# Optimization experiments

Hardware: AMD Instinct MI355X
Metric: run time of the kernel (lower is better)

## Reference

```python
import jax, jax.numpy as jnp
import numpy as np

B, T, I, H, O = 64, 2048, 128, 256, 1

def setup_inputs() -> dict:
    key = jax.random.key(0)
    ks = jax.random.split(key, 7)
    s = 0.05
    return {
        "x": jax.random.normal(ks[0], (B, T, I), jnp.float32),
        "W_ih": jax.random.normal(ks[1], (3 * H, I), jnp.float32) * s,
        "W_hh": jax.random.normal(ks[2], (3 * H, H), jnp.float32) * s,
        "b_ih": jax.random.normal(ks[3], (3 * H,), jnp.float32) * s,
        "b_hh": jax.random.normal(ks[4], (3 * H,), jnp.float32) * s,
        "W_o": jax.random.normal(ks[5], (O, H), jnp.float32) * s,
        "b_o": jax.random.normal(ks[6], (O,), jnp.float32) * s,
    }

def _gru_scan(x, W_ih, W_hh, b_ih, b_hh):
    # Precompute input projections for all timesteps: [T, B, 3H]
    gi = jnp.einsum('bti,gi->tbg', x, W_ih) + b_ih
    Hd = W_hh.shape[1]

    def step(h, gi_t):
        gh = h @ W_hh.T + b_hh  # [B, 3H]
        i_r, i_z, i_n = jnp.split(gi_t, 3, axis=-1)
        h_r, h_z, h_n = jnp.split(gh, 3, axis=-1)
        r = jax.nn.sigmoid(i_r + h_r)
        z = jax.nn.sigmoid(i_z + h_z)
        n = jnp.tanh(i_n + r * h_n)
        h_new = (1.0 - z) * n + z * h
        return h_new, h_new

    h0 = jnp.zeros((x.shape[0], Hd), x.dtype)
    _, hs = jax.lax.scan(step, h0, gi)  # hs: [T, B, H]
    return hs

def reference(x, W_ih, W_hh, b_ih, b_hh, W_o, b_o):
    hs = _gru_scan(x, W_ih, W_hh, b_ih, b_hh)        # [T, B, H]
    outputs = jnp.einsum('tbh,oh->bto', hs, W_o) + b_o  # [B, T, O], identity nonlinearity
    hiddens = jnp.transpose(hs, (1, 0, 2))              # [B, T, H]
    return outputs, hiddens
```

## Files before the change

### kernel.cpp

```cpp
#include <hip/hip_runtime.h>
#include <hip/hip_bf16.h>

#define BB 64
#define TT 2048
#define II 128
#define HH 256
#define GG 768

typedef _Float16 h2 __attribute__((ext_vector_type(2)));
typedef _Float16 half8 __attribute__((ext_vector_type(8)));
typedef float f32x4 __attribute__((ext_vector_type(4)));
union U32H2 { unsigned int u; h2 h; };

static __device__ __forceinline__ float fdot2f(unsigned int w, h2 hv, float acc){
#if __has_builtin(__builtin_amdgcn_fdot2)
    U32H2 c; c.u = w;
    return __builtin_amdgcn_fdot2(c.h, hv, acc, false);
#else
    U32H2 c; c.u = w;
    return acc + (float)c.h.x * (float)hv.x + (float)c.h.y * (float)hv.y;
#endif
}

__global__ void conv_whh(const float* __restrict__ Whh, unsigned int* __restrict__ Wt){
    int idx = blockIdx.x * 256 + threadIdx.x;
    int kk = idx / GG;
    int g  = idx - kk * GG;
    float a = Whh[g * HH + 2*kk];
    float b = Whh[g * HH + 2*kk + 1];
    U32H2 c; c.h.x = (_Float16)a; c.h.y = (_Float16)b;
    Wt[idx] = c.u;
}

__global__ void conv_wih(const float* __restrict__ Wih, _Float16* __restrict__ Wh){
    int idx = blockIdx.x * 256 + threadIdx.x;
    Wh[idx] = (_Float16)Wih[idx];
}

__global__ __launch_bounds__(256) void gi_mfma(const float* __restrict__ x,
                                               const _Float16* __restrict__ Wh,
                                               const float* __restrict__ bih,
                                               _Float16* __restrict__ gi){
    const int wave = threadIdx.x >> 6;
    const int lane = threadIdx.x & 63;
    const int l16  = lane & 15, q = lane >> 4;
    const int m    = blockIdx.x * 64 + wave * 16 + l16;
    const int n0   = blockIdx.y * 64;
    f32x4 acc[4] = {};
    #pragma unroll
    for (int s = 0; s < 4; ++s){
        const float* xp = x + (size_t)m * II + s*32 + q*8;
        float4 a0 = *(const float4*)xp;
        float4 a1 = *(const float4*)(xp + 4);
        half8 af = { (_Float16)a0.x,(_Float16)a0.y,(_Float16)a0.z,(_Float16)a0.w,
                     (_Float16)a1.x,(_Float16)a1.y,(_Float16)a1.z,(_Float16)a1.w };
        #pragma unroll
        for (int t = 0; t < 4; ++t){
            const _Float16* wp = Wh + (size_t)(n0 + t*16 + l16) * II + s*32 + q*8;
            half8 bf = *(const half8*)wp;
            acc[t] = __builtin_amdgcn_mfma_f32_16x16x32_f16(af, bf, acc[t], 0, 0, 0);
        }
    }
    #pragma unroll
    for (int t = 0; t < 4; ++t){
        int n = n0 + t*16 + l16;
        float bv = bih[n];
        #pragma unroll
        for (int r = 0; r < 4; ++r){
            int row = blockIdx.x*64 + wave*16 + q*4 + r;
            gi[(size_t)row * GG + n] = (_Float16)(acc[t][r] + bv);
        }
    }
}

__global__ __launch_bounds__(1024) void gru_rec(
        const unsigned int* __restrict__ Wt,
        const _Float16* __restrict__ gi,
        const float* __restrict__ bhh,
        float* __restrict__ hid)
{
    const int b   = blockIdx.x;
    const int tid = threadIdx.x;
    const int j   = tid & 255;
    const int q   = tid >> 8;

    unsigned int Wr[32], Wz[32], Wn[32];
    {
        const unsigned int* Wb = Wt + q * 32 * GG;
        #pragma unroll
        for (int m = 0; m < 32; ++m){
            Wr[m] = Wb[m * GG + j];
            Wz[m] = Wb[m * GG + j + 256];
            Wn[m] = Wb[m * GG + j + 512];
        }
    }
    float br = 0.f, bz = 0.f, bn = 0.f;
    if (q == 0){ br = bhh[j]; bz = bhh[j + 256]; bn = bhh[j + 512]; }

    __shared__ __align__(16) _Float16 hps[256];
    __shared__ float pbuf[3 * GG];
    if (tid < 256) hps[tid] = (_Float16)0.f;

    float h_prev = 0.f;
    const _Float16* gib = gi + (size_t)b * TT * GG;
    float* hob = hid + (size_t)b * TT * HH;
    __syncthreads();

    for (int t = 0; t < TT; ++t){
        float gir = 0.f, giz = 0.f, gin = 0.f;
        if (q == 0){
            const _Float16* g3 = gib + (size_t)t * GG + j;
            gir = (float)g3[0]; giz = (float)g3[256]; gin = (float)g3[512];
        }
        float ar = br, az = bz, an = bn;
        const uint4* hv = ((const uint4*)hps) + q * 8;
        #pragma unroll
        for (int mm = 0; mm < 8; ++mm){
            union { uint4 v; h2 p[4]; } hh;
            hh.v = hv[mm];
            #pragma unroll
            for (int p = 0; p < 4; ++p){
                ar = fdot2f(Wr[4*mm + p], hh.p[p], ar);
                az = fdot2f(Wz[4*mm + p], hh.p[p], az);
                an = fdot2f(Wn[4*mm + p], hh.p[p], an);
            }
        }
        if (q){
            float* pb = pbuf + (q - 1) * GG;
            pb[j] = ar; pb[j + 256] = az; pb[j + 512] = an;
        }
        __syncthreads();
        if (q == 0){
            ar += pbuf[j]       + pbuf[GG + j]       + pbuf[2*GG + j];
            az += pbuf[j + 256] + pbuf[GG + j + 256] + pbuf[2*GG + j + 256];
            an += pbuf[j + 512] + pbuf[GG + j + 512] + pbuf[2*GG + j + 512];
            float r = 1.f / (1.f + __expf(-(gir + ar)));
            float z = 1.f / (1.f + __expf(-(giz + az)));
            float tin = gin + r * an;
            tin = fminf(15.f, fmaxf(-15.f, tin));
            float e2 = __expf(2.f * tin);
            float n = (e2 - 1.f) / (e2 + 1.f);
            float hn = (1.f - z) * n + z * h_prev;
            h_prev = hn;
            hob[(size_t)t * HH + j] = hn;
            hps[j] = (_Float16)hn;
        }
        __syncthreads();
    }
}

__global__ __launch_bounds__(256) void out_proj(const float* __restrict__ hid,
                                                const float* __restrict__ Wo,
                                                const float* __restrict__ bo,
                                                float* __restrict__ outp){
    const int w = threadIdx.x >> 6, l = threadIdx.x & 63;
    const size_t bt = (size_t)blockIdx.x * 4 + w;
    const float4 hv = ((const float4*)(hid + bt * HH))[l];
    const float4 wv = ((const float4*)Wo)[l];
    float s = hv.x*wv.x + hv.y*wv.y + hv.z*wv.z + hv.w*wv.w;
    #pragma unroll
    for (int off = 32; off > 0; off >>= 1) s += __shfl_down(s, off, 64);
    if (l == 0) outp[bt] = s + bo[0];
}

extern "C" void kernel_launch(void* const* d_in, const int* in_sizes, int n_in,
                              void* d_out, int out_size, void* d_ws, size_t ws_size,
                              hipStream_t stream) {
    const float* x   = (const float*)d_in[0];
    const float* Wih = (const float*)d_in[1];
    const float* Whh = (const float*)d_in[2];
    const float* bih = (const float*)d_in[3];
    const float* bhh = (const float*)d_in[4];
    const float* Wo  = (const float*)d_in[5];
    const float* bo  = (const float*)d_in[6];

    float* outputs = (float*)d_out;
    float* hiddens = (float*)d_out + (size_t)BB * TT;

    unsigned int* Wt = (unsigned int*)d_ws;
    _Float16* Wh = (_Float16*)((char*)d_ws + 128 * GG * sizeof(unsigned int));
    _Float16* gi = (_Float16*)((char*)Wh + (size_t)GG * II * sizeof(_Float16));

    conv_whh<<<dim3(98304 / 256), dim3(256), 0, stream>>>(Whh, Wt);
    conv_wih<<<dim3(98304 / 256), dim3(256), 0, stream>>>(Wih, Wh);
    gi_mfma <<<dim3((BB * TT) / 64, GG / 64), dim3(256), 0, stream>>>(x, Wh, bih, gi);
    gru_rec <<<dim3(BB), dim3(1024), 0, stream>>>(Wt, gi, bhh, hiddens);
    out_proj<<<dim3((BB * TT) / 4), dim3(256), 0, stream>>>(hiddens, Wo, bo, outputs);
}
```

Measured before the change: 2.630 ms.

## Restructure GRU recurrence with shuffle reduction and double-buffered hidden state

The four K-partitions of each hidden unit now sit in adjacent lanes and are summed with xor-shuffles. This replaces the LDS partial-sum buffer and one of the two barriers per timestep, and every lane computes the gate math redundantly. The hidden vector is double-buffered in padded, replicated LDS copies so each partition reads its own bank-offset slice. The next step's gate input is prefetched a step ahead. The input-projection GEMM also widens each block to 192 output columns to reuse the converted x fragment. The trade-offs are more shuffles and redundant transcendental work per step, and higher register pressure in both kernels.

```diff
diff --git a/kernel.cpp b/kernel.cpp
--- a/kernel.cpp
+++ b/kernel.cpp
@@ -45,8 +45,8 @@
     const int lane = threadIdx.x & 63;
     const int l16  = lane & 15, q = lane >> 4;
     const int m    = blockIdx.x * 64 + wave * 16 + l16;
-    const int n0   = blockIdx.y * 64;
-    f32x4 acc[4] = {};
+    const int n0   = blockIdx.y * 192;
+    f32x4 acc[12] = {};
     #pragma unroll
     for (int s = 0; s < 4; ++s){
         const float* xp = x + (size_t)m * II + s*32 + q*8;
@@ -55,14 +55,14 @@
         half8 af = { (_Float16)a0.x,(_Float16)a0.y,(_Float16)a0.z,(_Float16)a0.w,
                      (_Float16)a1.x,(_Float16)a1.y,(_Float16)a1.z,(_Float16)a1.w };
         #pragma unroll
-        for (int t = 0; t < 4; ++t){
+        for (int t = 0; t < 12; ++t){
             const _Float16* wp = Wh + (size_t)(n0 + t*16 + l16) * II + s*32 + q*8;
             half8 bf = *(const half8*)wp;
             acc[t] = __builtin_amdgcn_mfma_f32_16x16x32_f16(af, bf, acc[t], 0, 0, 0);
         }
     }
     #pragma unroll
-    for (int t = 0; t < 4; ++t){
+    for (int t = 0; t < 12; ++t){
         int n = n0 + t*16 + l16;
         float bv = bih[n];
         #pragma unroll
@@ -73,7 +73,10 @@
     }
 }
 
-__global__ __launch_bounds__(1024) void gru_rec(
+#define HREP 272
+#define HBUF (4 * HREP)
+
+__global__ __launch_bounds__(1024, 4) void gru_rec(
         const unsigned int* __restrict__ Wt,
         const _Float16* __restrict__ gi,
         const float* __restrict__ bhh,
@@ -81,8 +84,8 @@
 {
     const int b   = blockIdx.x;
     const int tid = threadIdx.x;
-    const int j   = tid & 255;
-    const int q   = tid >> 8;
+    const int j   = tid >> 2;
+    const int q   = tid & 3;
 
     unsigned int Wr[32], Wz[32], Wn[32];
     {
@@ -94,30 +97,44 @@
             Wn[m] = Wb[m * GG + j + 512];
         }
     }
-    float br = 0.f, bz = 0.f, bn = 0.f;
-    if (q == 0){ br = bhh[j]; bz = bhh[j + 256]; bn = bhh[j + 512]; }
-
-    __shared__ __align__(16) _Float16 hps[256];
-    __shared__ float pbuf[3 * GG];
-    if (tid < 256) hps[tid] = (_Float16)0.f;
-
-    float h_prev = 0.f;
+    float bq = (q < 3) ? bhh[q * 256 + j] : 0.f;
+
+    __shared__ __align__(16) _Float16 hps[2 * HBUF];
+    for (int i = tid; i < 2 * HBUF; i += 1024) hps[i] = (_Float16)0.f;
+
     const _Float16* gib = gi + (size_t)b * TT * GG;
     float* hob = hid + (size_t)b * TT * HH;
+
+    float h_prev = 0.f;
+    _Float16 gcur = (q < 3) ? gib[q * 256 + j] : (_Float16)0.f;
+
+    const uint4* rd0 = (const uint4*)(hps + q * HREP + q * 64);
+    const uint4* rd1 = (const uint4*)(hps + HBUF + q * HREP + q * 64);
+    _Float16* wr0 = hps + q * HREP + j;
+    _Float16* wr1 = hps + HBUF + q * HREP + j;
+
     __syncthreads();
 
     for (int t = 0; t < TT; ++t){
-        float gir = 0.f, giz = 0.f, gin = 0.f;
-        if (q == 0){
-            const _Float16* g3 = gib + (size_t)t * GG + j;
-            gir = (float)g3[0]; giz = (float)g3[256]; gin = (float)g3[512];
-        }
-        float ar = br, az = bz, an = bn;
-        const uint4* hv = ((const uint4*)hps) + q * 8;
+        int tn = (t + 1 < TT) ? t + 1 : t;
+        _Float16 gnext = (q < 3) ? gib[(size_t)tn * GG + q * 256 + j]
+                                 : (_Float16)0.f;
+
+        const uint4* hv = (t & 1) ? rd1 : rd0;
+        uint4 hreg[8];
+        #pragma unroll
+        for (int mm = 0; mm < 8; ++mm) hreg[mm] = hv[mm];
+
+        float g = (float)gcur;
+        float ar = 0.f, az = 0.f, an = 0.f, gn = 0.f;
+        if      (q == 0) ar = bq + g;
+        else if (q == 1) az = bq + g;
+        else if (q == 2) { an = bq; gn = g; }
+
         #pragma unroll
         for (int mm = 0; mm < 8; ++mm){
             union { uint4 v; h2 p[4]; } hh;
-            hh.v = hv[mm];
+            hh.v = hreg[mm];
             #pragma unroll
             for (int p = 0; p < 4; ++p){
                 ar = fdot2f(Wr[4*mm + p], hh.p[p], ar);
@@ -125,26 +142,25 @@
                 an = fdot2f(Wn[4*mm + p], hh.p[p], an);
             }
         }
-        if (q){
-            float* pb = pbuf + (q - 1) * GG;
-            pb[j] = ar; pb[j + 256] = az; pb[j + 512] = an;
-        }
-        __syncthreads();
-        if (q == 0){
-            ar += pbuf[j]       + pbuf[GG + j]       + pbuf[2*GG + j];
-            az += pbuf[j + 256] + pbuf[GG + j + 256] + pbuf[2*GG + j + 256];
-            an += pbuf[j + 512] + pbuf[GG + j + 512] + pbuf[2*GG + j + 512];
-            float r = 1.f / (1.f + __expf(-(gir + ar)));
-            float z = 1.f / (1.f + __expf(-(giz + az)));
-            float tin = gin + r * an;
-            tin = fminf(15.f, fmaxf(-15.f, tin));
-            float e2 = __expf(2.f * tin);
-            float n = (e2 - 1.f) / (e2 + 1.f);
-            float hn = (1.f - z) * n + z * h_prev;
-            h_prev = hn;
-            hob[(size_t)t * HH + j] = hn;
-            hps[j] = (_Float16)hn;
-        }
+
+        ar += __shfl_xor(ar, 1); ar += __shfl_xor(ar, 2);
+        az += __shfl_xor(az, 1); az += __shfl_xor(az, 2);
+        an += __shfl_xor(an, 1); an += __shfl_xor(an, 2);
+        gn += __shfl_xor(gn, 1); gn += __shfl_xor(gn, 2);
+
+        float r = 1.f / (1.f + __expf(-ar));
+        float z = 1.f / (1.f + __expf(-az));
+        float tin = gn + r * an;
+        tin = fminf(15.f, fmaxf(-15.f, tin));
+        float e2 = __expf(2.f * tin);
+        float n = (e2 - 1.f) / (e2 + 1.f);
+        float hn = (1.f - z) * n + z * h_prev;
+        h_prev = hn;
+
+        *((t & 1) ? wr0 : wr1) = (_Float16)hn;
+        if (q == 3) hob[(size_t)t * HH + j] = hn;
+
+        gcur = gnext;
         __syncthreads();
     }
 }
@@ -183,7 +199,7 @@
 
     conv_whh<<<dim3(98304 / 256), dim3(256), 0, stream>>>(Whh, Wt);
     conv_wih<<<dim3(98304 / 256), dim3(256), 0, stream>>>(Wih, Wh);
-    gi_mfma <<<dim3((BB * TT) / 64, GG / 64), dim3(256), 0, stream>>>(x, Wh, bih, gi);
+    gi_mfma <<<dim3((BB * TT) / 64, GG / 192), dim3(256), 0, stream>>>(x, Wh, bih, gi);
     gru_rec <<<dim3(BB), dim3(1024), 0, stream>>>(Wt, gi, bhh, hiddens);
     out_proj<<<dim3((BB * TT) / 4), dim3(256), 0, stream>>>(hiddens, Wo, bo, outputs);
 }
```

Measured after the change: 7.963 ms. +202.8%, slower.
